# Optimization experiments

Hardware: AMD Instinct MI355X
Metric: run time of the kernel (lower is better)

The kernel has to match this reference:

```python
import jax, jax.numpy as jnp
import numpy as np

C = 512
H = 8

def setup_inputs() -> dict:
    key = jax.random.key(0)
    ks = jax.random.split(key, 5)
    x = jax.random.normal(ks[0], (4, C, 2048), dtype=jnp.float32)
    # Conv1d(kernel_size=1) == pointwise linear: weight [out, in], bias [out]
    qkv_w = jax.random.normal(ks[1], (3 * C, C), dtype=jnp.float32) * (1.0 / np.sqrt(C))
    qkv_b = jax.random.normal(ks[2], (3 * C,), dtype=jnp.float32) * 0.02
    proj_w = jax.random.normal(ks[3], (C, C), dtype=jnp.float32) * (1.0 / np.sqrt(C))
    proj_b = jax.random.normal(ks[4], (C,), dtype=jnp.float32) * 0.02
    return {"x": x, "qkv_w": qkv_w, "qkv_b": qkv_b, "proj_w": proj_w, "proj_b": proj_b}

def reference(x, qkv_w, qkv_b, proj_w, proj_b):
    b, c, t = x.shape
    scale = c ** (-0.5)  # NOTE: full channel count, matching the torch module
    # pointwise conv: [3C, C] @ [b, C, T] -> [b, 3C, T]
    qkv = jnp.einsum('oc,bct->bot', qkv_w, x) + qkv_b[None, :, None]
    q, k, v = jnp.split(qkv, 3, axis=1)
    d = c // H
    q = q.reshape(b, H, d, t)
    k = k.reshape(b, H, d, t)
    v = v.reshape(b, H, d, t)
    attn = jnp.einsum('bhct,bhcs->bhts', q, k) * scale
    attn = jax.nn.softmax(attn, axis=-1)
    out = jnp.einsum('bhts,bhcs->bhct', attn, v)
    out = out.reshape(b, c, t)
    out = jnp.einsum('oc,bct->bot', proj_w, out) + proj_b[None, :, None]
    return x + out
```

## Files before the change

kernel.cpp:

```cpp
#include <hip/hip_runtime.h>
#include <hip/hip_bf16.h>
#include <math.h>

#define B_DIM 4
#define C_DIM 512
#define T_DIM 2048
#define H_DIM 8
#define OC3   1536
#define VN_STRIDE 2064
#define SCALE 0.044194173824159216f
#define SCALE2 (0.044194173824159216f * 1.4426950408889634f)

typedef unsigned short ushortT;
typedef unsigned int uintT;
typedef __attribute__((ext_vector_type(8))) short bf16x8;
typedef __attribute__((ext_vector_type(4))) short bf16x4;
typedef __attribute__((ext_vector_type(4))) float f32x4;

__device__ __forceinline__ ushortT f2bf(float f) {
    union { float f; uintT u; } v; v.f = f;
    uintT r = v.u + 0x7FFF + ((v.u >> 16) & 1);
    return (ushortT)(r >> 16);
}
__device__ __forceinline__ float bf2f(ushortT h) {
    union { uintT u; float f; } v; v.u = ((uintT)h) << 16;
    return v.f;
}
__device__ __forceinline__ uintT pack2bf(float a, float b) {
    uintT ua = __float_as_uint(a) + 0x8000u;
    uintT ub = __float_as_uint(b) + 0x8000u;
    return (ua >> 16) | (ub & 0xFFFF0000u);
}
__device__ __forceinline__ uintT cvtpk2bf(float a, float b) {
    union { __bf16 v[2]; uintT u; } c;
    c.v[0] = (__bf16)a; c.v[1] = (__bf16)b;
    return c.u;
}
__device__ __forceinline__ void gload_lds16(const ushortT* g, ushortT* l) {
    __builtin_amdgcn_global_load_lds(
        (const __attribute__((address_space(1))) void*)g,
        (__attribute__((address_space(3))) void*)l, 16, 0, 0);
}

__global__ __launch_bounds__(256) void prep(const float* __restrict__ x,
                                            const float* __restrict__ qw,
                                            const float* __restrict__ pw,
                                            ushortT* __restrict__ xb,
                                            ushortT* __restrict__ qwb,
                                            ushortT* __restrict__ pwb) {
    __shared__ float xs[64][65];
    const int tid = threadIdx.x;
    const int blk = blockIdx.x;
    if (blk >= 1024) {
        int idx = ((blk - 1024) * 256 + tid) * 4;
        if (idx < OC3 * C_DIM) {
            float4 v = *(const float4*)(qw + idx);
            qwb[idx + 0] = f2bf(v.x); qwb[idx + 1] = f2bf(v.y);
            qwb[idx + 2] = f2bf(v.z); qwb[idx + 3] = f2bf(v.w);
        } else {
            idx -= OC3 * C_DIM;
            float4 v = *(const float4*)(pw + idx);
            pwb[idx + 0] = f2bf(v.x); pwb[idx + 1] = f2bf(v.y);
            pwb[idx + 2] = f2bf(v.z); pwb[idx + 3] = f2bf(v.w);
        }
        return;
    }
    const int b = blk >> 8, rem = blk & 255;
    const int c0 = (rem >> 5) * 64, t0 = (rem & 31) * 64;
    #pragma unroll
    for (int it = 0; it < 4; ++it) {
        int idx = it * 256 + tid;
        int r = idx >> 4, ch = idx & 15;
        float4 v = *(const float4*)(x + ((size_t)(b * C_DIM + c0 + r)) * T_DIM + t0 + ch * 4);
        xs[r][ch * 4 + 0] = v.x; xs[r][ch * 4 + 1] = v.y;
        xs[r][ch * 4 + 2] = v.z; xs[r][ch * 4 + 3] = v.w;
    }
    __syncthreads();
    #pragma unroll
    for (int it = 0; it < 2; ++it) {
        int idx = it * 256 + tid;
        int rt = idx >> 3, ch = idx & 7;
        union { ushortT s[8]; uint4 v; } tmp;
        #pragma unroll
        for (int k = 0; k < 8; ++k) tmp.s[k] = f2bf(xs[ch * 8 + k][rt]);
        *(uint4*)(xb + ((size_t)b * T_DIM + t0 + rt) * C_DIM + c0 + ch * 8) = tmp.v;
    }
}

__global__ __launch_bounds__(256, 2) void gemm_qkv(const ushortT* __restrict__ A,
                                                   const ushortT* __restrict__ Bw,
                                                   const float* __restrict__ bias,
                                                   ushortT* __restrict__ out,
                                                   ushortT* __restrict__ Vn) {
    __shared__ __align__(16) ushortT As[8192], Bs[8192];
    const int tid = threadIdx.x, lane = tid & 63, wid = tid >> 6;
    const int u = lane & 15, q = lane >> 4;
    const int wm = wid & 1, wn = wid >> 1;
    const int m0 = blockIdx.x * 128, n0 = blockIdx.y * 128;
    const int lrow = lane >> 2, lcol = (lane & 3) * 8;

    f32x4 acc[4][4];
    const f32x4 z = {0.f, 0.f, 0.f, 0.f};
    #pragma unroll
    for (int mi = 0; mi < 4; ++mi)
        #pragma unroll
        for (int ni = 0; ni < 4; ++ni) acc[mi][ni] = z;

    for (int k0 = 0; k0 < 512; k0 += 64) {
        __syncthreads();
        gload_lds16(A  + (size_t)(m0 + wid * 32 +      lrow) * 512 + k0      + lcol, &As[(wid * 32     ) * 32]);
        gload_lds16(A  + (size_t)(m0 + wid * 32 + 16 + lrow) * 512 + k0      + lcol, &As[(wid * 32 + 16) * 32]);
        gload_lds16(A  + (size_t)(m0 + wid * 32 +      lrow) * 512 + k0 + 32 + lcol, &As[4096 + (wid * 32     ) * 32]);
        gload_lds16(A  + (size_t)(m0 + wid * 32 + 16 + lrow) * 512 + k0 + 32 + lcol, &As[4096 + (wid * 32 + 16) * 32]);
        gload_lds16(Bw + (size_t)(n0 + wid * 32 +      lrow) * 512 + k0      + lcol, &Bs[(wid * 32     ) * 32]);
        gload_lds16(Bw + (size_t)(n0 + wid * 32 + 16 + lrow) * 512 + k0      + lcol, &Bs[(wid * 32 + 16) * 32]);
        gload_lds16(Bw + (size_t)(n0 + wid * 32 +      lrow) * 512 + k0 + 32 + lcol, &Bs[4096 + (wid * 32     ) * 32]);
        gload_lds16(Bw + (size_t)(n0 + wid * 32 + 16 + lrow) * 512 + k0 + 32 + lcol, &Bs[4096 + (wid * 32 + 16) * 32]);
        __syncthreads();
        bf16x8 af[4][2], bfr[4][2];
        #pragma unroll
        for (int mi = 0; mi < 4; ++mi) {
            af[mi][0] = *(const bf16x8*)&As[(wm * 64 + mi * 16 + u) * 32 + q * 8];
            af[mi][1] = *(const bf16x8*)&As[4096 + (wm * 64 + mi * 16 + u) * 32 + q * 8];
        }
        #pragma unroll
        for (int ni = 0; ni < 4; ++ni) {
            bfr[ni][0] = *(const bf16x8*)&Bs[(wn * 64 + ni * 16 + u) * 32 + q * 8];
            bfr[ni][1] = *(const bf16x8*)&Bs[4096 + (wn * 64 + ni * 16 + u) * 32 + q * 8];
        }
        #pragma unroll
        for (int mi = 0; mi < 4; ++mi)
            #pragma unroll
            for (int ni = 0; ni < 4; ++ni) {
                acc[mi][ni] = __builtin_amdgcn_mfma_f32_16x16x32_bf16(
                    af[mi][0], bfr[ni][0], acc[mi][ni], 0, 0, 0);
                acc[mi][ni] = __builtin_amdgcn_mfma_f32_16x16x32_bf16(
                    af[mi][1], bfr[ni][1], acc[mi][ni], 0, 0, 0);
            }
    }
    if (n0 < 1024) {
        const float scl = (n0 < 512) ? SCALE2 : 1.0f;
        #pragma unroll
        for (int ni = 0; ni < 4; ++ni) {
            int o = n0 + wn * 64 + ni * 16 + u;
            float bv = bias[o];
            #pragma unroll
            for (int mi = 0; mi < 4; ++mi)
                #pragma unroll
                for (int r = 0; r < 4; ++r) {
                    int m = m0 + wm * 64 + mi * 16 + q * 4 + r;
                    out[(size_t)m * OC3 + o] = f2bf((acc[mi][ni][r] + bv) * scl);
                }
        }
    } else {
        #pragma unroll
        for (int ni = 0; ni < 4; ++ni) {
            int o = n0 + wn * 64 + ni * 16 + u;
            float bv = bias[o];
            int oo = o - 1024;
            int hv = oo >> 6, d = oo & 63;
            #pragma unroll
            for (int mi = 0; mi < 4; ++mi) {
                int m = m0 + wm * 64 + mi * 16 + q * 4;
                int b = m >> 11, t = m & 2047;
                uint2 w;
                w.x = pack2bf(acc[mi][ni][0] + bv, acc[mi][ni][1] + bv);
                w.y = pack2bf(acc[mi][ni][2] + bv, acc[mi][ni][3] + bv);
                *(uint2*)(Vn + ((size_t)((b * 8 + hv) * 64 + d)) * VN_STRIDE + t) = w;
            }
        }
    }
}

__global__ __launch_bounds__(256, 2)
void flash(const ushortT* __restrict__ qkvT, const ushortT* __restrict__ Vn,
           ushortT* __restrict__ AO)
{
    __shared__ __align__(16) ushortT lds[4 * 4608];
    __shared__ float Lbuf[4][64];

    const int tid = threadIdx.x, lane = tid & 63, wid = tid >> 6;
    const int u = lane & 15, q = lane >> 4;
    const int gid = blockIdx.y * 32 + blockIdx.x;
    const int xg = gid >> 3;
    const int bh = (gid & 7) * 4 + (xg >> 5);
    const int tb = xg & 31;
    const int bb = bh >> 3, h = bh & 7;
    const int tblk = tb * 64;
    const size_t qbase = (size_t)bb * T_DIM * OC3;

    bf16x8 qb[4][2];
    #pragma unroll
    for (int ti = 0; ti < 4; ++ti)
        #pragma unroll
        for (int kst = 0; kst < 2; ++kst)
            qb[ti][kst] = *(const bf16x8*)(qkvT + qbase
                + (size_t)(tblk + ti * 16 + u) * OC3 + h * 64 + kst * 32 + q * 8);

    const ushortT* kp[4];
    #pragma unroll
    for (int si = 0; si < 4; ++si)
        kp[si] = qkvT + qbase + (size_t)(wid * 512 + si * 16 + u) * OC3 + 512 + h * 64;
    const ushortT* vp[4];
    #pragma unroll
    for (int ci = 0; ci < 4; ++ci)
        vp[ci] = Vn + ((size_t)bh * 64 + ci * 16 + u) * VN_STRIDE + wid * 512 + q * 4;

    f32x4 acc[4][4];
    const f32x4 z = {0.f, 0.f, 0.f, 0.f};
    #pragma unroll
    for (int ci = 0; ci < 4; ++ci)
        #pragma unroll
        for (int ti = 0; ti < 4; ++ti) acc[ci][ti] = z;
    f32x4 lacc[4] = {z, z, z, z};
    const bf16x4 ones = {(short)0x3F80, (short)0x3F80, (short)0x3F80, (short)0x3F80};

    for (int rnd = 0; rnd < 8; ++rnd) {
        bf16x8 ka[4][2];
        #pragma unroll
        for (int si = 0; si < 4; ++si) {
            ka[si][0] = *(const bf16x8*)(kp[si] + q * 8);
            ka[si][1] = *(const bf16x8*)(kp[si] + 32 + q * 8);
        }
        bf16x4 va[4][4];
        #pragma unroll
        for (int si = 0; si < 4; ++si)
            #pragma unroll
            for (int ci = 0; ci < 4; ++ci)
                va[si][ci] = *(const bf16x4*)(vp[ci] + si * 16);

        #pragma unroll
        for (int si = 0; si < 4; ++si) {
            f32x4 sacc[4] = {z, z, z, z};
            #pragma unroll
            for (int ti = 0; ti < 4; ++ti)
                sacc[ti] = __builtin_amdgcn_mfma_f32_16x16x32_bf16(
                    ka[si][0], qb[ti][0], sacc[ti], 0, 0, 0);
            #pragma unroll
            for (int ti = 0; ti < 4; ++ti)
                sacc[ti] = __builtin_amdgcn_mfma_f32_16x16x32_bf16(
                    ka[si][1], qb[ti][1], sacc[ti], 0, 0, 0);
            #pragma unroll
            for (int ti = 0; ti < 4; ++ti) {
                float p0 = __builtin_amdgcn_exp2f(sacc[ti][0]);
                float p1 = __builtin_amdgcn_exp2f(sacc[ti][1]);
                float p2 = __builtin_amdgcn_exp2f(sacc[ti][2]);
                float p3 = __builtin_amdgcn_exp2f(sacc[ti][3]);
                union { uint2 u2; bf16x4 v; } pw;
                pw.u2.x = cvtpk2bf(p0, p1);
                pw.u2.y = cvtpk2bf(p2, p3);
                lacc[ti] = __builtin_amdgcn_mfma_f32_16x16x16bf16_1k(
                    ones, pw.v, lacc[ti], 0, 0, 0);
                #pragma unroll
                for (int ci = 0; ci < 4; ++ci)
                    acc[ci][ti] = __builtin_amdgcn_mfma_f32_16x16x16bf16_1k(
                        va[si][ci], pw.v, acc[ci][ti], 0, 0, 0);
            }
        }
        #pragma unroll
        for (int si = 0; si < 4; ++si) kp[si] += 64 * OC3;
        #pragma unroll
        for (int ci = 0; ci < 4; ++ci) vp[ci] += 64;
    }

    ushortT* Ob = lds + wid * 4608;
    if (q == 0) {
        #pragma unroll
        for (int ti = 0; ti < 4; ++ti) Lbuf[wid][ti * 16 + u] = lacc[ti][0];
    }
    #pragma unroll
    for (int ci = 0; ci < 4; ++ci)
        #pragma unroll
        for (int ti = 0; ti < 4; ++ti) {
            uint2 w;
            w.x = pack2bf(acc[ci][ti][0], acc[ci][ti][1]);
            w.y = pack2bf(acc[ci][ti][2], acc[ci][ti][3]);
            *(uint2*)&Ob[(ti * 16 + u) * 72 + ci * 16 + q * 4] = w;
        }
    __syncthreads();
    {
        const int t = tid >> 2, cs = (tid & 3) * 16;
        float linv = 1.0f / (Lbuf[0][t] + Lbuf[1][t] + Lbuf[2][t] + Lbuf[3][t]);
        float vs[16];
        #pragma unroll
        for (int j = 0; j < 16; ++j) vs[j] = 0.f;
        #pragma unroll
        for (int w = 0; w < 4; ++w) {
            const ushortT* row = lds + w * 4608 + t * 72 + cs;
            #pragma unroll
            for (int j2 = 0; j2 < 2; ++j2) {
                uint4 rv = *(const uint4*)(row + j2 * 8);
                const uintT* rp = (const uintT*)&rv;
                #pragma unroll
                for (int k = 0; k < 4; ++k) {
                    vs[j2 * 8 + k * 2 + 0] += bf2f((ushortT)(rp[k] & 0xFFFF));
                    vs[j2 * 8 + k * 2 + 1] += bf2f((ushortT)(rp[k] >> 16));
                }
            }
        }
        uint4 o0, o1;
        uintT* op0 = (uintT*)&o0; uintT* op1 = (uintT*)&o1;
        #pragma unroll
        for (int k = 0; k < 4; ++k) {
            op0[k] = pack2bf(vs[k * 2] * linv, vs[k * 2 + 1] * linv);
            op1[k] = pack2bf(vs[8 + k * 2] * linv, vs[8 + k * 2 + 1] * linv);
        }
        size_t orow = ((size_t)bb * T_DIM + tblk + t) * C_DIM + h * 64 + cs;
        *(uint4*)(AO + orow) = o0;
        *(uint4*)(AO + orow + 8) = o1;
    }
}

__global__ __launch_bounds__(256, 2) void gemm_proj(const ushortT* __restrict__ Wp,
                                                    const ushortT* __restrict__ AOv,
                                                    const float* __restrict__ bias,
                                                    const float* __restrict__ xres,
                                                    float* __restrict__ out) {
    __shared__ __align__(16) ushortT As[8192], Bs[8192];
    const int tid = threadIdx.x, lane = tid & 63, wid = tid >> 6;
    const int u = lane & 15, q = lane >> 4;
    const int wm = wid & 1, wn = wid >> 1;
    const int m0 = blockIdx.y * 128, n0 = blockIdx.x * 128;
    const int lrow = lane >> 2, lcol = (lane & 3) * 8;

    f32x4 acc[4][4];
    const f32x4 z = {0.f, 0.f, 0.f, 0.f};
    #pragma unroll
    for (int mi = 0; mi < 4; ++mi)
        #pragma unroll
        for (int ni = 0; ni < 4; ++ni) acc[mi][ni] = z;

    for (int k0 = 0; k0 < 512; k0 += 64) {
        __syncthreads();
        gload_lds16(Wp  + (size_t)(m0 + wid * 32 +      lrow) * 512 + k0      + lcol, &As[(wid * 32     ) * 32]);
        gload_lds16(Wp  + (size_t)(m0 + wid * 32 + 16 + lrow) * 512 + k0      + lcol, &As[(wid * 32 + 16) * 32]);
        gload_lds16(Wp  + (size_t)(m0 + wid * 32 +      lrow) * 512 + k0 + 32 + lcol, &As[4096 + (wid * 32     ) * 32]);
        gload_lds16(Wp  + (size_t)(m0 + wid * 32 + 16 + lrow) * 512 + k0 + 32 + lcol, &As[4096 + (wid * 32 + 16) * 32]);
        gload_lds16(AOv + (size_t)(n0 + wid * 32 +      lrow) * 512 + k0      + lcol, &Bs[(wid * 32     ) * 32]);
        gload_lds16(AOv + (size_t)(n0 + wid * 32 + 16 + lrow) * 512 + k0      + lcol, &Bs[(wid * 32 + 16) * 32]);
        gload_lds16(AOv + (size_t)(n0 + wid * 32 +      lrow) * 512 + k0 + 32 + lcol, &Bs[4096 + (wid * 32     ) * 32]);
        gload_lds16(AOv + (size_t)(n0 + wid * 32 + 16 + lrow) * 512 + k0 + 32 + lcol, &Bs[4096 + (wid * 32 + 16) * 32]);
        __syncthreads();
        bf16x8 af[4][2], bfr[4][2];
        #pragma unroll
        for (int mi = 0; mi < 4; ++mi) {
            af[mi][0] = *(const bf16x8*)&As[(wm * 64 + mi * 16 + u) * 32 + q * 8];
            af[mi][1] = *(const bf16x8*)&As[4096 + (wm * 64 + mi * 16 + u) * 32 + q * 8];
        }
        #pragma unroll
        for (int ni = 0; ni < 4; ++ni) {
            bfr[ni][0] = *(const bf16x8*)&Bs[(wn * 64 + ni * 16 + u) * 32 + q * 8];
            bfr[ni][1] = *(const bf16x8*)&Bs[4096 + (wn * 64 + ni * 16 + u) * 32 + q * 8];
        }
        #pragma unroll
        for (int mi = 0; mi < 4; ++mi)
            #pragma unroll
            for (int ni = 0; ni < 4; ++ni) {
                acc[mi][ni] = __builtin_amdgcn_mfma_f32_16x16x32_bf16(
                    af[mi][0], bfr[ni][0], acc[mi][ni], 0, 0, 0);
                acc[mi][ni] = __builtin_amdgcn_mfma_f32_16x16x32_bf16(
                    af[mi][1], bfr[ni][1], acc[mi][ni], 0, 0, 0);
            }
    }
    #pragma unroll
    for (int mi = 0; mi < 4; ++mi)
        #pragma unroll
        for (int r = 0; r < 4; ++r) {
            int o = m0 + wm * 64 + mi * 16 + q * 4 + r;
            float bv = bias[o];
            #pragma unroll
            for (int ni = 0; ni < 4; ++ni) {
                int n = n0 + wn * 64 + ni * 16 + u;
                int b = n >> 11, t = n & 2047;
                size_t oi = ((size_t)b * C_DIM + o) * T_DIM + t;
                out[oi] = acc[mi][ni][r] + bv + xres[oi];
            }
        }
}

extern "C" void kernel_launch(void* const* d_in, const int* in_sizes, int n_in,
                              void* d_out, int out_size, void* d_ws, size_t ws_size,
                              hipStream_t stream)
{
    const float* x      = (const float*)d_in[0];
    const float* qkv_w  = (const float*)d_in[1];
    const float* qkv_b  = (const float*)d_in[2];
    const float* proj_w = (const float*)d_in[3];
    const float* proj_b = (const float*)d_in[4];
    float* out = (float*)d_out;

    char* ws = (char*)d_ws;
    ushortT* xb   = (ushortT*)(ws);
    ushortT* wqb  = (ushortT*)(ws +  8388608);
    ushortT* wpb  = (ushortT*)(ws +  9961472);
    ushortT* qkvT = (ushortT*)(ws + 10485760);
    ushortT* Vn   = (ushortT*)(ws + 35651584);
    ushortT* AO   = (ushortT*)(ws + 44105728);

    prep     <<<2048, 256, 0, stream>>>(x, qkv_w, proj_w, xb, wqb, wpb);
    gemm_qkv <<<dim3(64, 12),   256, 0, stream>>>(xb, wqb, qkv_b, qkvT, Vn);
    flash    <<<dim3(32, 32),   256, 0, stream>>>(qkvT, Vn, AO);
    gemm_proj<<<dim3(64, 4),    256, 0, stream>>>(wpb, AO, proj_b, x, out);
}
```

Measured before the change: 177.9 us.

## Restructure flash kernel to share K/V tiles via double-buffered LDS

The flash kernel now assigns 128 query rows per block, with each wave owning 32 queries. All waves iterate over the full key sequence using K/V tiles staged cooperatively into LDS through direct global-to-LDS loads, with double buffering and an XOR swizzle. Previously each wave streamed a disjoint quarter of keys straight from global memory and a cross-wave reduction combined partial results; now that reduction is gone and K/V global traffic per block is shared. It adds a barrier per key tile and halves the block count, so occupancy and latency hiding may suffer.

```diff
diff --git a/kernel.cpp b/kernel.cpp
--- a/kernel.cpp
+++ b/kernel.cpp
@@ -176,72 +176,88 @@
 void flash(const ushortT* __restrict__ qkvT, const ushortT* __restrict__ Vn,
            ushortT* __restrict__ AO)
 {
-    __shared__ __align__(16) ushortT lds[4 * 4608];
-    __shared__ float Lbuf[4][64];
+    __shared__ __align__(16) ushortT smem[16384];
 
     const int tid = threadIdx.x, lane = tid & 63, wid = tid >> 6;
     const int u = lane & 15, q = lane >> 4;
-    const int gid = blockIdx.y * 32 + blockIdx.x;
-    const int xg = gid >> 3;
-    const int bh = (gid & 7) * 4 + (xg >> 5);
-    const int tb = xg & 31;
+    const int g = blockIdx.x;
+    const int bh = (g & 7) * 4 + ((g >> 3) & 3);
+    const int qt = g >> 5;
     const int bb = bh >> 3, h = bh & 7;
-    const int tblk = tb * 64;
+    const int q0 = qt * 128;
     const size_t qbase = (size_t)bb * T_DIM * OC3;
 
-    bf16x8 qb[4][2];
-    #pragma unroll
-    for (int ti = 0; ti < 4; ++ti)
+    bf16x8 qb[2][2];
+    #pragma unroll
+    for (int ti = 0; ti < 2; ++ti)
         #pragma unroll
         for (int kst = 0; kst < 2; ++kst)
             qb[ti][kst] = *(const bf16x8*)(qkvT + qbase
-                + (size_t)(tblk + ti * 16 + u) * OC3 + h * 64 + kst * 32 + q * 8);
-
-    const ushortT* kp[4];
-    #pragma unroll
-    for (int si = 0; si < 4; ++si)
-        kp[si] = qkvT + qbase + (size_t)(wid * 512 + si * 16 + u) * OC3 + 512 + h * 64;
-    const ushortT* vp[4];
+                + (size_t)(q0 + wid * 32 + ti * 16 + u) * OC3 + h * 64 + kst * 32 + q * 8);
+
+    const int rs = wid * 8 + (lane >> 3);
+    const int sg = (lane & 7) ^ (rs & 7);
+    const ushortT* ks0 = qkvT + qbase + (size_t)(rs     ) * OC3 + 512 + h * 64 + sg * 8;
+    const ushortT* ks1 = qkvT + qbase + (size_t)(rs + 32) * OC3 + 512 + h * 64 + sg * 8;
+    const ushortT* vs0 = Vn + ((size_t)bh * 64 + rs     ) * VN_STRIDE + sg * 8;
+    const ushortT* vs1 = Vn + ((size_t)bh * 64 + rs + 32) * VN_STRIDE + sg * 8;
+
+    f32x4 acc[4][2];
+    const f32x4 z = {0.f, 0.f, 0.f, 0.f};
     #pragma unroll
     for (int ci = 0; ci < 4; ++ci)
-        vp[ci] = Vn + ((size_t)bh * 64 + ci * 16 + u) * VN_STRIDE + wid * 512 + q * 4;
-
-    f32x4 acc[4][4];
-    const f32x4 z = {0.f, 0.f, 0.f, 0.f};
-    #pragma unroll
-    for (int ci = 0; ci < 4; ++ci)
-        #pragma unroll
-        for (int ti = 0; ti < 4; ++ti) acc[ci][ti] = z;
-    f32x4 lacc[4] = {z, z, z, z};
+        #pragma unroll
+        for (int ti = 0; ti < 2; ++ti) acc[ci][ti] = z;
+    f32x4 lacc[2] = {z, z};
     const bf16x4 ones = {(short)0x3F80, (short)0x3F80, (short)0x3F80, (short)0x3F80};
 
-    for (int rnd = 0; rnd < 8; ++rnd) {
+    gload_lds16(ks0, &smem[       wid * 512]);
+    gload_lds16(ks1, &smem[2048 + wid * 512]);
+    gload_lds16(vs0, &smem[8192 +        wid * 512]);
+    gload_lds16(vs1, &smem[8192 + 2048 + wid * 512]);
+    ks0 += 64 * OC3; ks1 += 64 * OC3; vs0 += 64; vs1 += 64;
+    __syncthreads();
+
+    int cur = 0;
+    for (int rnd = 0; rnd < 32; ++rnd) {
+        if (rnd < 31) {
+            int nb = cur ^ 1;
+            gload_lds16(ks0, &smem[nb * 4096 +        wid * 512]);
+            gload_lds16(ks1, &smem[nb * 4096 + 2048 + wid * 512]);
+            gload_lds16(vs0, &smem[8192 + nb * 4096 +        wid * 512]);
+            gload_lds16(vs1, &smem[8192 + nb * 4096 + 2048 + wid * 512]);
+            ks0 += 64 * OC3; ks1 += 64 * OC3; vs0 += 64; vs1 += 64;
+        }
+        const ushortT* Kb = &smem[cur * 4096];
+        const ushortT* Vb = &smem[8192 + cur * 4096];
         bf16x8 ka[4][2];
         #pragma unroll
+        for (int si = 0; si < 4; ++si)
+            #pragma unroll
+            for (int kst = 0; kst < 2; ++kst)
+                ka[si][kst] = *(const bf16x8*)&Kb[(si * 16 + u) * 64
+                    + (((kst * 4 + q) ^ (u & 7)) * 8)];
+        bf16x4 va[4][4];
+        #pragma unroll
+        for (int si = 0; si < 4; ++si)
+            #pragma unroll
+            for (int ci = 0; ci < 4; ++ci)
+                va[si][ci] = *(const bf16x4*)&Vb[(ci * 16 + u) * 64
+                    + (((si * 2 + (q >> 1)) ^ (u & 7)) * 8) + (q & 1) * 4];
+
+        #pragma unroll
         for (int si = 0; si < 4; ++si) {
-            ka[si][0] = *(const bf16x8*)(kp[si] + q * 8);
-            ka[si][1] = *(const bf16x8*)(kp[si] + 32 + q * 8);
-        }
-        bf16x4 va[4][4];
-        #pragma unroll
-        for (int si = 0; si < 4; ++si)
-            #pragma unroll
-            for (int ci = 0; ci < 4; ++ci)
-                va[si][ci] = *(const bf16x4*)(vp[ci] + si * 16);
-
-        #pragma unroll
-        for (int si = 0; si < 4; ++si) {
-            f32x4 sacc[4] = {z, z, z, z};
-            #pragma unroll
-            for (int ti = 0; ti < 4; ++ti)
+            f32x4 sacc[2] = {z, z};
+            #pragma unroll
+            for (int ti = 0; ti < 2; ++ti)
                 sacc[ti] = __builtin_amdgcn_mfma_f32_16x16x32_bf16(
                     ka[si][0], qb[ti][0], sacc[ti], 0, 0, 0);
             #pragma unroll
-            for (int ti = 0; ti < 4; ++ti)
+            for (int ti = 0; ti < 2; ++ti)
                 sacc[ti] = __builtin_amdgcn_mfma_f32_16x16x32_bf16(
                     ka[si][1], qb[ti][1], sacc[ti], 0, 0, 0);
             #pragma unroll
-            for (int ti = 0; ti < 4; ++ti) {
+            for (int ti = 0; ti < 2; ++ti) {
                 float p0 = __builtin_amdgcn_exp2f(sacc[ti][0]);
                 float p1 = __builtin_amdgcn_exp2f(sacc[ti][1]);
                 float p2 = __builtin_amdgcn_exp2f(sacc[ti][2]);
@@ -257,21 +273,20 @@
                         va[si][ci], pw.v, acc[ci][ti], 0, 0, 0);
             }
         }
-        #pragma unroll
-        for (int si = 0; si < 4; ++si) kp[si] += 64 * OC3;
-        #pragma unroll
-        for (int ci = 0; ci < 4; ++ci) vp[ci] += 64;
-    }
-
-    ushortT* Ob = lds + wid * 4608;
+        __syncthreads();
+        cur ^= 1;
+    }
+
+    ushortT* Ob = smem + wid * 2304;
+    float* Lb = (float*)(smem + 9216);
     if (q == 0) {
-        #pragma unroll
-        for (int ti = 0; ti < 4; ++ti) Lbuf[wid][ti * 16 + u] = lacc[ti][0];
+        Lb[wid * 32 + u]      = lacc[0][0];
+        Lb[wid * 32 + 16 + u] = lacc[1][0];
     }
     #pragma unroll
     for (int ci = 0; ci < 4; ++ci)
         #pragma unroll
-        for (int ti = 0; ti < 4; ++ti) {
+        for (int ti = 0; ti < 2; ++ti) {
             uint2 w;
             w.x = pack2bf(acc[ci][ti][0], acc[ci][ti][1]);
             w.y = pack2bf(acc[ci][ti][2], acc[ci][ti][3]);
@@ -279,35 +294,23 @@
         }
     __syncthreads();
     {
-        const int t = tid >> 2, cs = (tid & 3) * 16;
-        float linv = 1.0f / (Lbuf[0][t] + Lbuf[1][t] + Lbuf[2][t] + Lbuf[3][t]);
-        float vs[16];
-        #pragma unroll
-        for (int j = 0; j < 16; ++j) vs[j] = 0.f;
-        #pragma unroll
-        for (int w = 0; w < 4; ++w) {
-            const ushortT* row = lds + w * 4608 + t * 72 + cs;
-            #pragma unroll
-            for (int j2 = 0; j2 < 2; ++j2) {
-                uint4 rv = *(const uint4*)(row + j2 * 8);
-                const uintT* rp = (const uintT*)&rv;
-                #pragma unroll
-                for (int k = 0; k < 4; ++k) {
-                    vs[j2 * 8 + k * 2 + 0] += bf2f((ushortT)(rp[k] & 0xFFFF));
-                    vs[j2 * 8 + k * 2 + 1] += bf2f((ushortT)(rp[k] >> 16));
-                }
-            }
-        }
-        uint4 o0, o1;
-        uintT* op0 = (uintT*)&o0; uintT* op1 = (uintT*)&o1;
-        #pragma unroll
-        for (int k = 0; k < 4; ++k) {
-            op0[k] = pack2bf(vs[k * 2] * linv, vs[k * 2 + 1] * linv);
-            op1[k] = pack2bf(vs[8 + k * 2] * linv, vs[8 + k * 2 + 1] * linv);
-        }
-        size_t orow = ((size_t)bb * T_DIM + tblk + t) * C_DIM + h * 64 + cs;
-        *(uint4*)(AO + orow) = o0;
-        *(uint4*)(AO + orow + 8) = o1;
+        const int row = tid >> 1, cs = (tid & 1) * 32;
+        const int w = row >> 5, r32 = row & 31;
+        float linv = 1.0f / Lb[w * 32 + r32];
+        const ushortT* rp = smem + w * 2304 + r32 * 72 + cs;
+        size_t orow = ((size_t)bb * T_DIM + q0 + row) * C_DIM + h * 64 + cs;
+        #pragma unroll
+        for (int j = 0; j < 4; ++j) {
+            uint4 rv = *(const uint4*)(rp + j * 8);
+            const uintT* rpp = (const uintT*)&rv;
+            uint4 o;
+            uintT* op = (uintT*)&o;
+            #pragma unroll
+            for (int k = 0; k < 4; ++k)
+                op[k] = pack2bf(bf2f((ushortT)(rpp[k] & 0xFFFF)) * linv,
+                                bf2f((ushortT)(rpp[k] >> 16)) * linv);
+            *(uint4*)(AO + orow + j * 8) = o;
+        }
     }
 }
 
@@ -399,6 +402,6 @@
 
     prep     <<<2048, 256, 0, stream>>>(x, qkv_w, proj_w, xb, wqb, wpb);
     gemm_qkv <<<dim3(64, 12),   256, 0, stream>>>(xb, wqb, qkv_b, qkvT, Vn);
-    flash    <<<dim3(32, 32),   256, 0, stream>>>(qkvT, Vn, AO);
+    flash    <<<512,            256, 0, stream>>>(qkvT, Vn, AO);
     gemm_proj<<<dim3(64, 4),    256, 0, stream>>>(wpb, AO, proj_b, x, out);
 }
```

Result: faster. 158.8 us (-10.7%).
